# Kernel tuning notes

Hardware: AMD Instinct MI355X
Metric: run time of the kernel (lower is better)

## Reference

```python
import jax, jax.numpy as jnp
import numpy as np

HEADS = 16
D_MODEL = 2048
HEAD_DIM = D_MODEL // HEADS


def setup_inputs() -> dict:
    key = jax.random.key(0)
    ks = jax.random.split(key, 8)
    s = 1.0 / np.sqrt(D_MODEL)
    return {
        "hidden_states": jax.random.normal(ks[0], (2, 2048, D_MODEL), jnp.float32),
        "Wq": jax.random.normal(ks[1], (D_MODEL, D_MODEL), jnp.float32) * s,
        "bq": jax.random.normal(ks[2], (D_MODEL,), jnp.float32) * s,
        "Wk": jax.random.normal(ks[3], (D_MODEL, D_MODEL), jnp.float32) * s,
        "Wv": jax.random.normal(ks[4], (D_MODEL, D_MODEL), jnp.float32) * s,
        "bv": jax.random.normal(ks[5], (D_MODEL,), jnp.float32) * s,
        "Wo": jax.random.normal(ks[6], (D_MODEL, D_MODEL), jnp.float32) * s,
        "bo": jax.random.normal(ks[7], (D_MODEL,), jnp.float32) * s,
    }


def reference(hidden_states, Wq, bq, Wk, Wv, bv, Wo, bo):
    bsz, q_len, _ = hidden_states.shape
    # torch Linear: y = x @ W^T + b; k_W has no bias
    q = hidden_states @ Wq.T + bq
    k = hidden_states @ Wk.T
    v = hidden_states @ Wv.T + bv
    # [b, h, s, d]
    def split_heads(t):
        return t.reshape(bsz, q_len, HEADS, HEAD_DIM).transpose(0, 2, 1, 3)
    q, k, v = split_heads(q), split_heads(k), split_heads(v)
    scale = 1.0 / np.sqrt(HEAD_DIM).astype(np.float32)
    attn_weights = jnp.einsum("bhqd,bhkd->bhqk", q, k) * scale
    attn_weights = jax.nn.softmax(attn_weights, axis=-1)
    attn_output = jnp.einsum("bhqk,bhkd->bhqd", attn_weights, v)
    attn_output = attn_output.transpose(0, 2, 1, 3).reshape(bsz, q_len, D_MODEL)
    attn_output = attn_output @ Wo.T + bo
    return attn_output, attn_weights
```

## Files before the change

### kernel.cpp

```cpp
#include <hip/hip_runtime.h>

typedef _Float16 f16;
typedef _Float16 f16x4 __attribute__((ext_vector_type(4)));
typedef _Float16 f16x8 __attribute__((ext_vector_type(8)));
typedef float f32x4 __attribute__((ext_vector_type(4)));

#define DM 2048
#define NT 4096
#define SEQ 2048
#define HD 128
#define NBH 32
#define QSCALE (0.08838834764831845f * 1.4426950408889634f)

__device__ __forceinline__ void gload16(const f16* g, f16* l) {
  __builtin_amdgcn_global_load_lds(
      (const __attribute__((address_space(1))) void*)g,
      (__attribute__((address_space(3))) void*)l, 16, 0, 0);
}

#define LGKM0                                        \
  asm volatile("s_waitcnt lgkmcnt(0)" ::: "memory"); \
  __builtin_amdgcn_sched_barrier(0)
#define VMC6                                       \
  asm volatile("s_waitcnt vmcnt(6)" ::: "memory"); \
  __builtin_amdgcn_sched_barrier(0)
#define VMC4                                       \
  asm volatile("s_waitcnt vmcnt(4)" ::: "memory"); \
  __builtin_amdgcn_sched_barrier(0)
#define VMC0                                       \
  asm volatile("s_waitcnt vmcnt(0)" ::: "memory"); \
  __builtin_amdgcn_sched_barrier(0)

__global__ __launch_bounds__(256) void cvt_f32_f16(const float* __restrict__ src,
                                                   f16* __restrict__ dst, int n4) {
  int i = blockIdx.x * 256 + threadIdx.x;
  int st = gridDim.x * 256;
  for (; i < n4; i += st) {
    float4 v = ((const float4*)src)[i];
    f16x4 h = {(f16)v.x, (f16)v.y, (f16)v.z, (f16)v.w};
    ((f16x4*)dst)[i] = h;
  }
}

__global__ __launch_bounds__(256) void cvt4_f32_f16(const float* __restrict__ hs,
                                                    const float* __restrict__ s0,
                                                    const float* __restrict__ s1,
                                                    const float* __restrict__ s2,
                                                    f16* __restrict__ hsd,
                                                    f16* __restrict__ wd) {
  int i = blockIdx.x * 256 + threadIdx.x;
  int st = gridDim.x * 256;
  for (; i < 5 * 1048576; i += st) {
    float4 v;
    f16x4 h;
    if (i < 2 * 1048576) {
      v = ((const float4*)hs)[i];
      h[0] = (f16)v.x; h[1] = (f16)v.y; h[2] = (f16)v.z; h[3] = (f16)v.w;
      ((f16x4*)hsd)[i] = h;
    } else {
      const int j = i - 2 * 1048576;
      const int r = j >> 20, jj = j & 1048575;
      const float* s = (r == 0) ? s0 : ((r == 1) ? s1 : s2);
      v = ((const float4*)s)[jj];
      h[0] = (f16)v.x; h[1] = (f16)v.y; h[2] = (f16)v.z; h[3] = (f16)v.w;
      ((f16x4*)wd)[j] = h;
    }
  }
}

template <int MODE>
__global__ __launch_bounds__(512, 2) void gemm8(const f16* __restrict__ A,
                                                const f16* __restrict__ Bm,
                                                const float* __restrict__ bias1,
                                                const float* __restrict__ bias2,
                                                float* __restrict__ outF,
                                                f16* __restrict__ outQ,
                                                f16* __restrict__ outK,
                                                f16* __restrict__ outV) {
  __shared__ __align__(16) f16 smem[73728];
  const int tid = threadIdx.x;
  const int w = tid >> 6, l = tid & 63;
  const int wr = w >> 2, wc = w & 3;
  const int sl = l & 15, t4 = l >> 4;

  const int nbx = gridDim.x, nby = gridDim.y;
  const int flat = blockIdx.y * nbx + blockIdx.x;
  const int chunk = (nbx * nby) >> 3;
  const int swz = (flat & 7) * chunk + (flat >> 3);
  const int col0 = (swz / nby) * 256, row0 = (swz % nby) * 128;

  f32x4 acc[4][4] = {};

  const int sr8 = l >> 3;
  const int sch = (l & 7) ^ (sr8 & 7);
  const f16* gA0 = A + (size_t)(row0 + w * 8 + sr8) * DM + sch * 8;
  const f16* gB0 = Bm + (size_t)(col0 + w * 8 + sr8) * DM + sch * 8;

#define SA(tb, kt, r) \
  gload16(gA0 + (size_t)(r) * 64 * DM + (kt) * 64, smem + (tb) * 8192 + (r) * 4096 + w * 512)
#define SB(tb, kt, r)                               \
  gload16(gB0 + (size_t)(r) * 64 * DM + (kt) * 64, \
          smem + 24576 + (tb) * 16384 + (r) * 4096 + w * 512)
#define MF(mi, ni, av, bv) \
  acc[mi][ni] = __builtin_amdgcn_mfma_f32_16x16x32_f16(av, bv, acc[mi][ni], 0, 0, 0)

  const int sx = sl & 7;
  const int sk0 = (t4 ^ sx) * 8;
  const int sk1 = ((4 + t4) ^ sx) * 8;
  const int arow = (wr * 64 + sl) * 64;
  const int brow = (wc * 64 + sl) * 64;

  SA(0, 0, 0); SA(0, 0, 1);
  SB(0, 0, 0); SB(0, 0, 1); SB(0, 0, 2); SB(0, 0, 3);
  SA(1, 1, 0); SA(1, 1, 1);
  SB(1, 1, 0); SB(1, 1, 1); SB(1, 1, 2); SB(1, 1, 3);
  VMC6;
  __builtin_amdgcn_s_barrier();

  int cur = 0;
#pragma unroll 1
  for (int t = 0; t < 32; ++t) {
    const int nb = (cur == 0) ? 2 : cur - 1;
    const bool pf = (t + 2 < 32);
    const int ab = cur * 8192;
    const int bb = 24576 + cur * 16384;
    f16x8 b0, b1, b2, b3, a0, a1;

    b0 = *(const f16x8*)&smem[bb + brow + sk0];
    b1 = *(const f16x8*)&smem[bb + brow + 1024 + sk0];
    b2 = *(const f16x8*)&smem[bb + brow + 2048 + sk0];
    b3 = *(const f16x8*)&smem[bb + brow + 3072 + sk0];
    a0 = *(const f16x8*)&smem[ab + arow + sk0];
    a1 = *(const f16x8*)&smem[ab + arow + 1024 + sk0];
    if (pf) { SA(nb, t + 2, 0); SA(nb, t + 2, 1); }
    __builtin_amdgcn_s_barrier();
    LGKM0;
    __builtin_amdgcn_s_setprio(1);
    MF(0, 0, a0, b0); MF(0, 1, a0, b1); MF(0, 2, a0, b2); MF(0, 3, a0, b3);
    MF(1, 0, a1, b0); MF(1, 1, a1, b1); MF(1, 2, a1, b2); MF(1, 3, a1, b3);
    __builtin_amdgcn_s_setprio(0);
    __builtin_amdgcn_s_barrier();

    a0 = *(const f16x8*)&smem[ab + arow + 2048 + sk0];
    a1 = *(const f16x8*)&smem[ab + arow + 3072 + sk0];
    if (pf) { SB(nb, t + 2, 0); SB(nb, t + 2, 1); }
    __builtin_amdgcn_s_barrier();
    LGKM0;
    __builtin_amdgcn_s_setprio(1);
    MF(2, 0, a0, b0); MF(2, 1, a0, b1); MF(2, 2, a0, b2); MF(2, 3, a0, b3);
    MF(3, 0, a1, b0); MF(3, 1, a1, b1); MF(3, 2, a1, b2); MF(3, 3, a1, b3);
    __builtin_amdgcn_s_setprio(0);
    __builtin_amdgcn_s_barrier();

    b0 = *(const f16x8*)&smem[bb + brow + sk1];
    b1 = *(const f16x8*)&smem[bb + brow + 1024 + sk1];
    b2 = *(const f16x8*)&smem[bb + brow + 2048 + sk1];
    b3 = *(const f16x8*)&smem[bb + brow + 3072 + sk1];
    a0 = *(const f16x8*)&smem[ab + arow + sk1];
    a1 = *(const f16x8*)&smem[ab + arow + 1024 + sk1];
    if (pf) { SB(nb, t + 2, 2); SB(nb, t + 2, 3); }
    __builtin_amdgcn_s_barrier();
    LGKM0;
    __builtin_amdgcn_s_setprio(1);
    MF(0, 0, a0, b0); MF(0, 1, a0, b1); MF(0, 2, a0, b2); MF(0, 3, a0, b3);
    MF(1, 0, a1, b0); MF(1, 1, a1, b1); MF(1, 2, a1, b2); MF(1, 3, a1, b3);
    __builtin_amdgcn_s_setprio(0);
    __builtin_amdgcn_s_barrier();

    a0 = *(const f16x8*)&smem[ab + arow + 2048 + sk1];
    a1 = *(const f16x8*)&smem[ab + arow + 3072 + sk1];
    __builtin_amdgcn_s_barrier();
    LGKM0;
    __builtin_amdgcn_s_setprio(1);
    MF(2, 0, a0, b0); MF(2, 1, a0, b1); MF(2, 2, a0, b2); MF(2, 3, a0, b3);
    MF(3, 0, a1, b0); MF(3, 1, a1, b1); MF(3, 2, a1, b2); MF(3, 3, a1, b3);
    __builtin_amdgcn_s_setprio(0);
    if (t < 30) { VMC6; } else { VMC0; }
    __builtin_amdgcn_s_barrier();
    cur = (cur == 2) ? 0 : cur + 1;
  }
#undef SA
#undef SB
#undef MF

  const int rl0 = wr * 64 + t4 * 4;
  const int cl0 = wc * 64 + sl;
  if constexpr (MODE == 0) {
#pragma unroll
    for (int mi = 0; mi < 4; mi++) {
#pragma unroll
      for (int ni = 0; ni < 4; ni++) {
        const int col = col0 + cl0 + ni * 16;
        const float bi = bias1[col];
#pragma unroll
        for (int j = 0; j < 4; j++) {
          const int row = row0 + rl0 + mi * 16 + j;
          __builtin_nontemporal_store(acc[mi][ni][j] + bi, &outF[(size_t)row * DM + col]);
        }
      }
    }
  } else {
    const int region = col0 >> 11;
    const int c2 = col0 & 2047;
    __syncthreads();
    if (region == 2) {
#pragma unroll
      for (int mi = 0; mi < 4; mi++)
#pragma unroll
        for (int ni = 0; ni < 4; ni++) {
          const int cl = cl0 + ni * 16;
          const float bb2 = bias2[c2 + cl];
#pragma unroll
          for (int j = 0; j < 4; j++)
            smem[cl * 136 + rl0 + mi * 16 + j] = (f16)(acc[mi][ni][j] + bb2);
        }
      __syncthreads();
      const int b = row0 >> 11, s0 = row0 & 2047;
#pragma unroll
      for (int it = 0; it < 8; ++it) {
        const int ck = it * 512 + tid;
        const int ci = ck >> 4, cc = (ck & 15) * 8;
        const int dg = c2 + ci;
        *(f16x8*)&outV[((size_t)(b * 16 + (dg >> 7)) * HD + (dg & 127)) * SEQ + s0 + cc] =
            *(const f16x8*)&smem[ci * 136 + cc];
      }
    } else {
#pragma unroll
      for (int mi = 0; mi < 4; mi++)
#pragma unroll
        for (int ni = 0; ni < 4; ni++) {
          const int cl = cl0 + ni * 16;
          const int cg = c2 + cl;
          const float badd = (region == 0) ? bias1[cg] : 0.0f;
#pragma unroll
          for (int j = 0; j < 4; j++) {
            float v = acc[mi][ni][j] + badd;
            if (region == 0) v *= QSCALE;
            smem[(rl0 + mi * 16 + j) * 264 + cl] = (f16)v;
          }
        }
      __syncthreads();
      f16* const dst = (region == 0 ? outQ : outK) + (size_t)row0 * DM + c2;
#pragma unroll
      for (int it = 0; it < 8; ++it) {
        const int ck = it * 512 + tid;
        const int rr = ck >> 5, cc = (ck & 31) * 8;
        *(f16x8*)&dst[(size_t)rr * DM + cc] = *(const f16x8*)&smem[rr * 264 + cc];
      }
    }
  }
}

__global__ __launch_bounds__(256, 2) void attn(const f16* __restrict__ Q,
                                               const f16* __restrict__ Kt,
                                               const f16* __restrict__ Vt,
                                               float* __restrict__ Pout,
                                               f16* __restrict__ Oout) {
  __shared__ __align__(16) f16 smem[36864];
  f16* const lP = smem + 32768;

  const int tid = threadIdx.x, w = tid >> 6, l = tid & 63;
  const int t = l >> 4, sl = l & 15, t8 = l >> 3, sl8 = l & 7;

  const int flat = blockIdx.y * gridDim.x + blockIdx.x;
  const int swz = (flat & 7) * 128 + (flat >> 3);
  const int bh = swz >> 5, q0 = (swz & 31) * 64;

  const int b = bh >> 4, h = bh & 15;
  const f16* Qg = Q + (size_t)(b * SEQ) * DM + h * HD;
  const f16* Kg = Kt + (size_t)(b * SEQ) * DM + h * HD;
  const f16* Vg = Vt + (size_t)bh * HD * SEQ;

#pragma unroll
  for (int c = 0; c < 4; c++) {
    const int row = w * 16 + c * 4 + t;
    const int ch = sl ^ (row & 7);
    gload16(Qg + (size_t)(q0 + row) * DM + ch * 8, smem + 16384 + w * 2048 + c * 512);
    gload16(Kg + (size_t)row * DM + ch * 8, smem + w * 2048 + c * 512);
    gload16(Kg + (size_t)(64 + row) * DM + ch * 8, smem + 8192 + w * 2048 + c * 512);
  }
  __syncthreads();

  f16x8 qf[4];
  {
    const int row = w * 16 + sl;
#pragma unroll
    for (int g = 0; g < 4; g++) {
      const int ch = (g * 4 + t) ^ (row & 7);
      qf[g] = *(const f16x8*)&smem[16384 + row * 128 + ch * 8];
    }
  }
  LGKM0;
  __builtin_amdgcn_s_barrier();

  float lsum = 0.0f;

  for (int kb = 0; kb < 32; ++kb) {
    f16* const kc = smem + (kb & 3) * 8192;
    if (kb + 2 < 32) {
      f16* const kn = smem + ((kb + 2) & 3) * 8192;
#pragma unroll
      for (int c = 0; c < 4; c++) {
        const int row = w * 16 + c * 4 + t;
        const int ch = sl ^ (row & 7);
        gload16(Kg + (size_t)((kb + 2) * 64 + row) * DM + ch * 8, kn + w * 2048 + c * 512);
      }
    }
#pragma unroll
    for (int cb = 0; cb < 4; ++cb) {
      f32x4 s = {0.f, 0.f, 0.f, 0.f};
      const int key = cb * 16 + sl;
#pragma unroll
      for (int g = 0; g < 4; ++g) {
        const int ch = (g * 4 + t) ^ (key & 7);
        f16x8 kf = *(const f16x8*)&kc[key * 128 + ch * 8];
        s = __builtin_amdgcn_mfma_f32_16x16x32_f16(kf, qf[g], s, 0, 0, 0);
      }
#pragma unroll
      for (int j = 0; j < 4; j++) lsum += __builtin_amdgcn_exp2f(s[j]);
    }
    if (kb < 31) {
      if (kb + 2 < 32) { VMC4; } else { VMC0; }
      __builtin_amdgcn_s_barrier();
    }
  }
  lsum += __shfl_xor(lsum, 16);
  lsum += __shfl_xor(lsum, 32);
  const float inv = 1.0f / lsum;

  {
#pragma unroll
    for (int c = 0; c < 4; c++) {
      const int row = w * 16 + c * 4 + t;
      const int ch = sl ^ (row & 7);
      gload16(Kg + (size_t)row * DM + ch * 8, smem + w * 2048 + c * 512);
    }
#pragma unroll
    for (int c = 0; c < 4; c++) {
      const int row = w * 32 + c * 8 + t8;
      const int ch = sl8 ^ (row & 7);
      gload16(Vg + (size_t)row * SEQ + ch * 8, smem + 16384 + w * 2048 + c * 512);
    }
  }
  __syncthreads();

  f32x4 oacc[8] = {};
  const int qrow = w * 16 + sl;
  float* const Prow = Pout + ((size_t)bh * SEQ + q0 + qrow) * SEQ;

  for (int kb = 0; kb < 32; ++kb) {
    f16* const kc = smem + (kb & 1) * 8192;
    f16* const vc = smem + 16384 + (kb & 1) * 8192;
    if (kb < 31) {
      f16* const kn = smem + ((kb + 1) & 1) * 8192;
      f16* const vn = smem + 16384 + ((kb + 1) & 1) * 8192;
#pragma unroll
      for (int c = 0; c < 4; c++) {
        const int row = w * 16 + c * 4 + t;
        const int ch = sl ^ (row & 7);
        gload16(Kg + (size_t)((kb + 1) * 64 + row) * DM + ch * 8, kn + w * 2048 + c * 512);
      }
#pragma unroll
      for (int c = 0; c < 4; c++) {
        const int row = w * 32 + c * 8 + t8;
        const int ch = sl8 ^ (row & 7);
        gload16(Vg + (size_t)row * SEQ + (kb + 1) * 64 + ch * 8, vn + w * 2048 + c * 512);
      }
    }
#pragma unroll
    for (int cb = 0; cb < 4; ++cb) {
      f32x4 s = {0.f, 0.f, 0.f, 0.f};
      const int key = cb * 16 + sl;
#pragma unroll
      for (int g = 0; g < 4; ++g) {
        const int ch = (g * 4 + t) ^ (key & 7);
        f16x8 kf = *(const f16x8*)&kc[key * 128 + ch * 8];
        s = __builtin_amdgcn_mfma_f32_16x16x32_f16(kf, qf[g], s, 0, 0, 0);
      }
      f32x4 p4;
      f16x4 ph;
#pragma unroll
      for (int j = 0; j < 4; j++) {
        const float p = __builtin_amdgcn_exp2f(s[j]) * inv;
        p4[j] = p;
        ph[j] = (f16)p;
      }
      __builtin_nontemporal_store(p4, (f32x4*)(Prow + kb * 64 + cb * 16 + t * 4));
      const int chs = (cb * 2 + (t >> 1)) ^ (qrow & 7);
      *(f16x4*)&lP[qrow * 64 + chs * 8 + (t & 1) * 4] = ph;
    }
    f16x8 pf[2];
#pragma unroll
    for (int ks = 0; ks < 2; ++ks) {
      const int ch = (ks * 4 + t) ^ (qrow & 7);
      pf[ks] = *(const f16x8*)&lP[qrow * 64 + ch * 8];
    }
    __builtin_amdgcn_s_setprio(1);
#pragma unroll
    for (int cb = 0; cb < 8; ++cb) {
      const int d = cb * 16 + sl;
#pragma unroll
      for (int ks = 0; ks < 2; ++ks) {
        const int ch = (ks * 4 + t) ^ (d & 7);
        f16x8 vf = *(const f16x8*)&vc[d * 64 + ch * 8];
        oacc[cb] = __builtin_amdgcn_mfma_f32_16x16x32_f16(pf[ks], vf, oacc[cb], 0, 0, 0);
      }
    }
    __builtin_amdgcn_s_setprio(0);
    if (kb < 31) {
      VMC4;
      __builtin_amdgcn_s_barrier();
    }
  }

#pragma unroll
  for (int cb = 0; cb < 8; ++cb) {
    const int d = cb * 16 + sl;
#pragma unroll
    for (int j = 0; j < 4; j++) {
      const int lrow = w * 16 + t * 4 + j;
      Oout[((size_t)(b * SEQ + q0 + lrow)) * DM + h * HD + d] = (f16)oacc[cb][j];
    }
  }
}

extern "C" void kernel_launch(void* const* d_in, const int* in_sizes, int n_in,
                              void* d_out, int out_size, void* d_ws, size_t ws_size,
                              hipStream_t stream) {
  const float* hs = (const float*)d_in[0];
  const float* Wq = (const float*)d_in[1];
  const float* bq = (const float*)d_in[2];
  const float* Wk = (const float*)d_in[3];
  const float* Wv = (const float*)d_in[4];
  const float* bv = (const float*)d_in[5];
  const float* Wo = (const float*)d_in[6];
  const float* bo = (const float*)d_in[7];
  float* out = (float*)d_out;
  float* Pout = out + (size_t)NT * DM;

  f16* q16 = (f16*)d_ws;
  f16* k16 = q16 + (size_t)NT * DM;
  f16* vt16 = k16 + (size_t)NT * DM;
  f16* ao16 = vt16 + (size_t)NT * DM;
  f16* hs16 = (f16*)Pout;
  f16* wqkv16 = hs16 + (size_t)NT * DM;
  f16* wo16 = q16;

  cvt4_f32_f16<<<2048, 256, 0, stream>>>(hs, Wq, Wk, Wv, hs16, wqkv16);

  gemm8<3><<<dim3(6144 / 256, NT / 128), 512, 0, stream>>>(
      hs16, wqkv16, bq, bv, nullptr, q16, k16, vt16);

  attn<<<dim3(SEQ / 64, NBH), 256, 0, stream>>>(q16, k16, vt16, Pout, ao16);

  cvt_f32_f16<<<1024, 256, 0, stream>>>(Wo, wo16, DM * DM / 4);
  gemm8<0><<<dim3(DM / 256, NT / 128), 512, 0, stream>>>(
      ao16, wo16, bo, nullptr, out, nullptr, nullptr, nullptr);
}
```

Baseline: 380.0 us.

## Software-pipeline PV matmul one block behind QK and fold Wo conversion into first cvt

The second attention pass now issues the V tile load for the current block and the K load for the next block, then runs the P·V MFMAs for the previous block, so the V load has a full iteration to land and the exp/store work overlaps the PV math. A final epilogue drains the last PV block. Separately, when the workspace is large enough, Wo is converted to fp16 in the same launch as the other inputs, which removes one kernel launch. The cost is extra registers for the carried P fragments and a dependence on the workspace size check.

```diff
diff --git a/kernel.cpp b/kernel.cpp
--- a/kernel.cpp
+++ b/kernel.cpp
@@ -42,15 +42,14 @@
   }
 }
 
-__global__ __launch_bounds__(256) void cvt4_f32_f16(const float* __restrict__ hs,
-                                                    const float* __restrict__ s0,
-                                                    const float* __restrict__ s1,
-                                                    const float* __restrict__ s2,
-                                                    f16* __restrict__ hsd,
-                                                    f16* __restrict__ wd) {
+__global__ __launch_bounds__(256) void cvt5_f32_f16(
+    const float* __restrict__ hs, const float* __restrict__ s0,
+    const float* __restrict__ s1, const float* __restrict__ s2,
+    const float* __restrict__ s3, f16* __restrict__ hsd, f16* __restrict__ wd,
+    f16* __restrict__ wod, int n4) {
   int i = blockIdx.x * 256 + threadIdx.x;
   int st = gridDim.x * 256;
-  for (; i < 5 * 1048576; i += st) {
+  for (; i < n4; i += st) {
     float4 v;
     f16x4 h;
     if (i < 2 * 1048576) {
@@ -60,10 +59,11 @@
     } else {
       const int j = i - 2 * 1048576;
       const int r = j >> 20, jj = j & 1048575;
-      const float* s = (r == 0) ? s0 : ((r == 1) ? s1 : s2);
+      const float* s = (r == 0) ? s0 : ((r == 1) ? s1 : ((r == 2) ? s2 : s3));
       v = ((const float4*)s)[jj];
       h[0] = (f16)v.x; h[1] = (f16)v.y; h[2] = (f16)v.z; h[3] = (f16)v.w;
-      ((f16x4*)wd)[j] = h;
+      if (r < 3) ((f16x4*)wd)[j] = h;
+      else ((f16x4*)wod)[jj] = h;
     }
   }
 }
@@ -295,6 +295,7 @@
 
   float lsum = 0.0f;
 
+#pragma unroll 1
   for (int kb = 0; kb < 32; ++kb) {
     f16* const kc = smem + (kb & 3) * 8192;
     if (kb + 2 < 32) {
@@ -328,45 +329,39 @@
   lsum += __shfl_xor(lsum, 32);
   const float inv = 1.0f / lsum;
 
-  {
-#pragma unroll
-    for (int c = 0; c < 4; c++) {
-      const int row = w * 16 + c * 4 + t;
-      const int ch = sl ^ (row & 7);
-      gload16(Kg + (size_t)row * DM + ch * 8, smem + w * 2048 + c * 512);
-    }
+#pragma unroll
+  for (int c = 0; c < 4; c++) {
+    const int row = w * 16 + c * 4 + t;
+    const int ch = sl ^ (row & 7);
+    gload16(Kg + (size_t)row * DM + ch * 8, smem + w * 2048 + c * 512);
+  }
+  VMC0;
+  __builtin_amdgcn_s_barrier();
+
+  f32x4 oacc[8] = {};
+  const int qrow = w * 16 + sl;
+  float* const Prow = Pout + ((size_t)bh * SEQ + q0 + qrow) * SEQ;
+  f16x8 pfp0, pfp1;
+
+#pragma unroll 1
+  for (int kb = 0; kb < 32; ++kb) {
 #pragma unroll
     for (int c = 0; c < 4; c++) {
       const int row = w * 32 + c * 8 + t8;
       const int ch = sl8 ^ (row & 7);
-      gload16(Vg + (size_t)row * SEQ + ch * 8, smem + 16384 + w * 2048 + c * 512);
-    }
-  }
-  __syncthreads();
-
-  f32x4 oacc[8] = {};
-  const int qrow = w * 16 + sl;
-  float* const Prow = Pout + ((size_t)bh * SEQ + q0 + qrow) * SEQ;
-
-  for (int kb = 0; kb < 32; ++kb) {
-    f16* const kc = smem + (kb & 1) * 8192;
-    f16* const vc = smem + 16384 + (kb & 1) * 8192;
-    if (kb < 31) {
-      f16* const kn = smem + ((kb + 1) & 1) * 8192;
-      f16* const vn = smem + 16384 + ((kb + 1) & 1) * 8192;
+      gload16(Vg + (size_t)row * SEQ + kb * 64 + ch * 8,
+              smem + 16384 + (kb & 1) * 8192 + w * 2048 + c * 512);
+    }
+    if (kb + 1 < 32) {
 #pragma unroll
       for (int c = 0; c < 4; c++) {
         const int row = w * 16 + c * 4 + t;
         const int ch = sl ^ (row & 7);
-        gload16(Kg + (size_t)((kb + 1) * 64 + row) * DM + ch * 8, kn + w * 2048 + c * 512);
-      }
-#pragma unroll
-      for (int c = 0; c < 4; c++) {
-        const int row = w * 32 + c * 8 + t8;
-        const int ch = sl8 ^ (row & 7);
-        gload16(Vg + (size_t)row * SEQ + (kb + 1) * 64 + ch * 8, vn + w * 2048 + c * 512);
-      }
-    }
+        gload16(Kg + (size_t)((kb + 1) * 64 + row) * DM + ch * 8,
+                smem + ((kb + 1) & 1) * 8192 + w * 2048 + c * 512);
+      }
+    }
+    f16* const kc = smem + (kb & 1) * 8192;
 #pragma unroll
     for (int cb = 0; cb < 4; ++cb) {
       f32x4 s = {0.f, 0.f, 0.f, 0.f};
@@ -389,28 +384,38 @@
       const int chs = (cb * 2 + (t >> 1)) ^ (qrow & 7);
       *(f16x4*)&lP[qrow * 64 + chs * 8 + (t & 1) * 4] = ph;
     }
-    f16x8 pf[2];
-#pragma unroll
-    for (int ks = 0; ks < 2; ++ks) {
-      const int ch = (ks * 4 + t) ^ (qrow & 7);
-      pf[ks] = *(const f16x8*)&lP[qrow * 64 + ch * 8];
-    }
+    f16x8 pfn0 = *(const f16x8*)&lP[qrow * 64 + ((t ^ (qrow & 7)) * 8)];
+    f16x8 pfn1 = *(const f16x8*)&lP[qrow * 64 + (((4 + t) ^ (qrow & 7)) * 8)];
+    if (kb > 0) {
+      f16* const vc = smem + 16384 + ((kb - 1) & 1) * 8192;
+      __builtin_amdgcn_s_setprio(1);
+#pragma unroll
+      for (int db = 0; db < 8; ++db) {
+        const int d = db * 16 + sl;
+        f16x8 vf0 = *(const f16x8*)&vc[d * 64 + ((t ^ (d & 7)) * 8)];
+        f16x8 vf1 = *(const f16x8*)&vc[d * 64 + (((4 + t) ^ (d & 7)) * 8)];
+        oacc[db] = __builtin_amdgcn_mfma_f32_16x16x32_f16(pfp0, vf0, oacc[db], 0, 0, 0);
+        oacc[db] = __builtin_amdgcn_mfma_f32_16x16x32_f16(pfp1, vf1, oacc[db], 0, 0, 0);
+      }
+      __builtin_amdgcn_s_setprio(0);
+    }
+    pfp0 = pfn0;
+    pfp1 = pfn1;
+    VMC4;
+    __builtin_amdgcn_s_barrier();
+  }
+  {
+    f16* const vc = smem + 16384 + 8192;
     __builtin_amdgcn_s_setprio(1);
 #pragma unroll
-    for (int cb = 0; cb < 8; ++cb) {
-      const int d = cb * 16 + sl;
-#pragma unroll
-      for (int ks = 0; ks < 2; ++ks) {
-        const int ch = (ks * 4 + t) ^ (d & 7);
-        f16x8 vf = *(const f16x8*)&vc[d * 64 + ch * 8];
-        oacc[cb] = __builtin_amdgcn_mfma_f32_16x16x32_f16(pf[ks], vf, oacc[cb], 0, 0, 0);
-      }
+    for (int db = 0; db < 8; ++db) {
+      const int d = db * 16 + sl;
+      f16x8 vf0 = *(const f16x8*)&vc[d * 64 + ((t ^ (d & 7)) * 8)];
+      f16x8 vf1 = *(const f16x8*)&vc[d * 64 + (((4 + t) ^ (d & 7)) * 8)];
+      oacc[db] = __builtin_amdgcn_mfma_f32_16x16x32_f16(pfp0, vf0, oacc[db], 0, 0, 0);
+      oacc[db] = __builtin_amdgcn_mfma_f32_16x16x32_f16(pfp1, vf1, oacc[db], 0, 0, 0);
     }
     __builtin_amdgcn_s_setprio(0);
-    if (kb < 31) {
-      VMC4;
-      __builtin_amdgcn_s_barrier();
-    }
   }
 
 #pragma unroll
@@ -444,16 +449,19 @@
   f16* ao16 = vt16 + (size_t)NT * DM;
   f16* hs16 = (f16*)Pout;
   f16* wqkv16 = hs16 + (size_t)NT * DM;
-  f16* wo16 = q16;
-
-  cvt4_f32_f16<<<2048, 256, 0, stream>>>(hs, Wq, Wk, Wv, hs16, wqkv16);
+
+  const bool bigws = ws_size >= (size_t)72 * 1024 * 1024 + 65536;
+  f16* wo16 = bigws ? (ao16 + (size_t)NT * DM) : q16;
+
+  cvt5_f32_f16<<<2048, 256, 0, stream>>>(hs, Wq, Wk, Wv, Wo, hs16, wqkv16, wo16,
+                                         bigws ? 6 * 1048576 : 5 * 1048576);
 
   gemm8<3><<<dim3(6144 / 256, NT / 128), 512, 0, stream>>>(
       hs16, wqkv16, bq, bv, nullptr, q16, k16, vt16);
 
   attn<<<dim3(SEQ / 64, NBH), 256, 0, stream>>>(q16, k16, vt16, Pout, ao16);
 
-  cvt_f32_f16<<<1024, 256, 0, stream>>>(Wo, wo16, DM * DM / 4);
+  if (!bigws) cvt_f32_f16<<<1024, 256, 0, stream>>>(Wo, wo16, DM * DM / 4);
   gemm8<0><<<dim3(DM / 256, NT / 128), 512, 0, stream>>>(
       ao16, wo16, bo, nullptr, out, nullptr, nullptr, nullptr);
 }
```

Measured after the change: 381.9 us. About the same (+0.5%).

## Split attention into row-sum and output kernels, fold Wo conversion into first cast

Applied to the files above, without the earlier changes.

Splits the two-pass attention kernel into a first kernel that computes only the softmax denominators, using 3-stage K buffering and a smaller LDS footprint for higher occupancy, and a second kernel that reads them back to emit P and the output. The inverse row sums go to scratch space in the output buffer. When the workspace is large enough, the Wo fp32-to-fp16 conversion is merged into the initial cast kernel, which removes one launch. This adds a kernel launch and an extra global round trip for the row sums, and it reloads Q in the second kernel.

```diff
diff --git a/kernel.cpp b/kernel.cpp
--- a/kernel.cpp
+++ b/kernel.cpp
@@ -42,15 +42,14 @@
   }
 }
 
-__global__ __launch_bounds__(256) void cvt4_f32_f16(const float* __restrict__ hs,
-                                                    const float* __restrict__ s0,
-                                                    const float* __restrict__ s1,
-                                                    const float* __restrict__ s2,
-                                                    f16* __restrict__ hsd,
-                                                    f16* __restrict__ wd) {
+__global__ __launch_bounds__(256) void cvt5_f32_f16(
+    const float* __restrict__ hs, const float* __restrict__ s0,
+    const float* __restrict__ s1, const float* __restrict__ s2,
+    const float* __restrict__ s3, f16* __restrict__ hsd, f16* __restrict__ wd,
+    f16* __restrict__ wod, int n4) {
   int i = blockIdx.x * 256 + threadIdx.x;
   int st = gridDim.x * 256;
-  for (; i < 5 * 1048576; i += st) {
+  for (; i < n4; i += st) {
     float4 v;
     f16x4 h;
     if (i < 2 * 1048576) {
@@ -60,10 +59,11 @@
     } else {
       const int j = i - 2 * 1048576;
       const int r = j >> 20, jj = j & 1048575;
-      const float* s = (r == 0) ? s0 : ((r == 1) ? s1 : s2);
+      const float* s = (r == 0) ? s0 : ((r == 1) ? s1 : ((r == 2) ? s2 : s3));
       v = ((const float4*)s)[jj];
       h[0] = (f16)v.x; h[1] = (f16)v.y; h[2] = (f16)v.z; h[3] = (f16)v.w;
-      ((f16x4*)wd)[j] = h;
+      if (r < 3) ((f16x4*)wd)[j] = h;
+      else ((f16x4*)wod)[jj] = h;
     }
   }
 }
@@ -251,16 +251,12 @@
   }
 }
 
-__global__ __launch_bounds__(256, 2) void attn(const f16* __restrict__ Q,
-                                               const f16* __restrict__ Kt,
-                                               const f16* __restrict__ Vt,
-                                               float* __restrict__ Pout,
-                                               f16* __restrict__ Oout) {
-  __shared__ __align__(16) f16 smem[36864];
-  f16* const lP = smem + 32768;
-
+__global__ __launch_bounds__(256, 3) void attn_p1(const f16* __restrict__ Q,
+                                                  const f16* __restrict__ Kt,
+                                                  float* __restrict__ invg) {
+  __shared__ __align__(16) f16 smem[24576];
   const int tid = threadIdx.x, w = tid >> 6, l = tid & 63;
-  const int t = l >> 4, sl = l & 15, t8 = l >> 3, sl8 = l & 7;
+  const int t = l >> 4, sl = l & 15;
 
   const int flat = blockIdx.y * gridDim.x + blockIdx.x;
   const int swz = (flat & 7) * 128 + (flat >> 3);
@@ -269,7 +265,6 @@
   const int b = bh >> 4, h = bh & 15;
   const f16* Qg = Q + (size_t)(b * SEQ) * DM + h * HD;
   const f16* Kg = Kt + (size_t)(b * SEQ) * DM + h * HD;
-  const f16* Vg = Vt + (size_t)bh * HD * SEQ;
 
 #pragma unroll
   for (int c = 0; c < 4; c++) {
@@ -294,11 +289,12 @@
   __builtin_amdgcn_s_barrier();
 
   float lsum = 0.0f;
-
+  int cur = 0;
+#pragma unroll 1
   for (int kb = 0; kb < 32; ++kb) {
-    f16* const kc = smem + (kb & 3) * 8192;
+    f16* const kc = smem + cur * 8192;
     if (kb + 2 < 32) {
-      f16* const kn = smem + ((kb + 2) & 3) * 8192;
+      f16* const kn = smem + ((cur == 0) ? 2 : cur - 1) * 8192;
 #pragma unroll
       for (int c = 0; c < 4; c++) {
         const int row = w * 16 + c * 4 + t;
@@ -323,31 +319,67 @@
       if (kb + 2 < 32) { VMC4; } else { VMC0; }
       __builtin_amdgcn_s_barrier();
     }
+    cur = (cur == 2) ? 0 : cur + 1;
   }
   lsum += __shfl_xor(lsum, 16);
   lsum += __shfl_xor(lsum, 32);
-  const float inv = 1.0f / lsum;
-
-  {
-#pragma unroll
-    for (int c = 0; c < 4; c++) {
-      const int row = w * 16 + c * 4 + t;
-      const int ch = sl ^ (row & 7);
-      gload16(Kg + (size_t)row * DM + ch * 8, smem + w * 2048 + c * 512);
-    }
-#pragma unroll
-    for (int c = 0; c < 4; c++) {
-      const int row = w * 32 + c * 8 + t8;
-      const int ch = sl8 ^ (row & 7);
-      gload16(Vg + (size_t)row * SEQ + ch * 8, smem + 16384 + w * 2048 + c * 512);
-    }
+  if (t == 0) invg[(size_t)bh * SEQ + q0 + w * 16 + sl] = 1.0f / lsum;
+}
+
+__global__ __launch_bounds__(256, 2) void attn_p2(const f16* __restrict__ Q,
+                                                  const f16* __restrict__ Kt,
+                                                  const f16* __restrict__ Vt,
+                                                  const float* __restrict__ invg,
+                                                  float* __restrict__ Pout,
+                                                  f16* __restrict__ Oout) {
+  __shared__ __align__(16) f16 smem[36864];
+  f16* const lP = smem + 32768;
+
+  const int tid = threadIdx.x, w = tid >> 6, l = tid & 63;
+  const int t = l >> 4, sl = l & 15, t8 = l >> 3, sl8 = l & 7;
+
+  const int flat = blockIdx.y * gridDim.x + blockIdx.x;
+  const int swz = (flat & 7) * 128 + (flat >> 3);
+  const int bh = swz >> 5, q0 = (swz & 31) * 64;
+
+  const int b = bh >> 4, h = bh & 15;
+  const f16* Qg = Q + (size_t)(b * SEQ) * DM + h * HD;
+  const f16* Kg = Kt + (size_t)(b * SEQ) * DM + h * HD;
+  const f16* Vg = Vt + (size_t)bh * HD * SEQ;
+
+#pragma unroll
+  for (int c = 0; c < 4; c++) {
+    const int row = w * 16 + c * 4 + t;
+    const int ch = sl ^ (row & 7);
+    gload16(Qg + (size_t)(q0 + row) * DM + ch * 8, smem + 16384 + w * 2048 + c * 512);
+    gload16(Kg + (size_t)row * DM + ch * 8, smem + w * 2048 + c * 512);
   }
   __syncthreads();
 
+  const int qrow = w * 16 + sl;
+  f16x8 qf[4];
+#pragma unroll
+  for (int g = 0; g < 4; g++) {
+    const int ch = (g * 4 + t) ^ (qrow & 7);
+    qf[g] = *(const f16x8*)&smem[16384 + qrow * 128 + ch * 8];
+  }
+  const float inv = invg[(size_t)bh * SEQ + q0 + qrow];
+  LGKM0;
+  __builtin_amdgcn_s_barrier();
+
+#pragma unroll
+  for (int c = 0; c < 4; c++) {
+    const int row = w * 32 + c * 8 + t8;
+    const int ch = sl8 ^ (row & 7);
+    gload16(Vg + (size_t)row * SEQ + ch * 8, smem + 16384 + w * 2048 + c * 512);
+  }
+  VMC0;
+  __builtin_amdgcn_s_barrier();
+
   f32x4 oacc[8] = {};
-  const int qrow = w * 16 + sl;
   float* const Prow = Pout + ((size_t)bh * SEQ + q0 + qrow) * SEQ;
 
+#pragma unroll 1
   for (int kb = 0; kb < 32; ++kb) {
     f16* const kc = smem + (kb & 1) * 8192;
     f16* const vc = smem + 16384 + (kb & 1) * 8192;
@@ -437,6 +469,7 @@
   const float* bo = (const float*)d_in[7];
   float* out = (float*)d_out;
   float* Pout = out + (size_t)NT * DM;
+  float* invg = out;
 
   f16* q16 = (f16*)d_ws;
   f16* k16 = q16 + (size_t)NT * DM;
@@ -444,16 +477,20 @@
   f16* ao16 = vt16 + (size_t)NT * DM;
   f16* hs16 = (f16*)Pout;
   f16* wqkv16 = hs16 + (size_t)NT * DM;
-  f16* wo16 = q16;
-
-  cvt4_f32_f16<<<2048, 256, 0, stream>>>(hs, Wq, Wk, Wv, hs16, wqkv16);
+
+  const bool bigws = ws_size >= (size_t)72 * 1024 * 1024 + 65536;
+  f16* wo16 = bigws ? (ao16 + (size_t)NT * DM) : q16;
+
+  cvt5_f32_f16<<<2048, 256, 0, stream>>>(hs, Wq, Wk, Wv, Wo, hs16, wqkv16, wo16,
+                                         bigws ? 6 * 1048576 : 5 * 1048576);
 
   gemm8<3><<<dim3(6144 / 256, NT / 128), 512, 0, stream>>>(
       hs16, wqkv16, bq, bv, nullptr, q16, k16, vt16);
 
-  attn<<<dim3(SEQ / 64, NBH), 256, 0, stream>>>(q16, k16, vt16, Pout, ao16);
-
-  cvt_f32_f16<<<1024, 256, 0, stream>>>(Wo, wo16, DM * DM / 4);
+  attn_p1<<<dim3(SEQ / 64, NBH), 256, 0, stream>>>(q16, k16, invg);
+  attn_p2<<<dim3(SEQ / 64, NBH), 256, 0, stream>>>(q16, k16, vt16, invg, Pout, ao16);
+
+  if (!bigws) cvt_f32_f16<<<1024, 256, 0, stream>>>(Wo, wo16, DM * DM / 4);
   gemm8<0><<<dim3(DM / 256, NT / 128), 512, 0, stream>>>(
       ao16, wo16, bo, nullptr, out, nullptr, nullptr, nullptr);
 }
```

Result: slower. 393.3 us (+3.5%).
